# Performance work log

Measured on AMD Instinct MI355X. Metric: run time of the kernel, lower is better.

The kernel has to match this reference:

```python
import jax, jax.numpy as jnp
import numpy as np

K = 3  # dynamic filter kernel size
EPS = 1e-10


def _filter_norm_spatial(s, std_param):
    # s: (B, K*K, H, W); normalize over filter-tap dim (unbiased std, as torch)
    s = s - s.mean(axis=1, keepdims=True)
    s = s / (s.std(axis=1, keepdims=True, ddof=1) + EPS)
    return s * std_param[None, :, None, None]


def _filter_norm_channel(cf, std_param, B, C):
    # cf: (B, C*K*K); normalize over the K*K taps of each channel
    cf = cf.reshape(B, C, K * K)
    cf = cf - cf.mean(axis=2, keepdims=True)
    cf = cf / (cf.std(axis=2, keepdims=True, ddof=1) + EPS)
    cf = cf.reshape(B, C * K * K) * std_param[None, :]
    return cf.reshape(B, C, K * K)


def _ddf_pack(x, sw, sb, sstd, cw1, cb1, cw2, cb2, cstd):
    B, C, H, W = x.shape
    # spatial branch: 1x1 conv -> per-pixel K*K spatial filter
    s = jnp.einsum('bchw,oc->bohw', x, sw) + sb[None, :, None, None]
    s = _filter_norm_spatial(s, sstd)                      # (B, 9, H, W)
    # channel branch: GAP -> SE MLP -> per-channel K*K filter
    g = x.mean(axis=(2, 3))                                # (B, C)
    h = jax.nn.relu(g @ cw1.T + cb1)                       # (B, mid)
    cf = h @ cw2.T + cb2                                   # (B, C*9)
    cf = _filter_norm_channel(cf, cstd, B, C)              # (B, C, 9)
    # apply decoupled dynamic filter: w[b,c,uv,h,w] = cf[b,c,uv] * s[b,uv,h,w]
    pad = K // 2
    xp = jnp.pad(x, ((0, 0), (0, 0), (pad, pad), (pad, pad)))
    # patches: (B, C, 9, H, W) -- the 9 shifted views (unfold)
    patches = jnp.stack([xp[:, :, i:i + H, j:j + W]
                         for i in range(K) for j in range(K)], axis=2)
    return jnp.einsum('bckhw,bck,bkhw->bchw', patches, cf, s)


def setup_inputs() -> dict:
    key = jax.random.key(0)
    ks = jax.random.split(key, 20)
    nf, mid = 64, 12
    std_scale = np.sqrt(2.0) / K  # calculate_gain('relu') / kernel_size
    d = {'x': jax.random.normal(ks[0], (4, nf, 256, 256), jnp.float32)}
    i = 1
    for p in ('1', '2'):
        d['sw' + p] = jax.random.normal(ks[i], (K * K, nf), jnp.float32) * 0.1; i += 1
        d['sb' + p] = jax.random.normal(ks[i], (K * K,), jnp.float32) * 0.1; i += 1
        d['sstd' + p] = jax.random.normal(ks[i], (K * K,), jnp.float32) * std_scale; i += 1
        d['cw1_' + p] = jax.random.normal(ks[i], (mid, nf), jnp.float32) * 0.1; i += 1
        d['cb1_' + p] = jax.random.normal(ks[i], (mid,), jnp.float32) * 0.1; i += 1
        d['cw2_' + p] = jax.random.normal(ks[i], (nf * K * K, mid), jnp.float32) * 0.1; i += 1
        d['cb2_' + p] = jax.random.normal(ks[i], (nf * K * K,), jnp.float32) * 0.1; i += 1
        d['cstd' + p] = jax.random.normal(ks[i], (nf * K * K,), jnp.float32) * std_scale; i += 1
    return d


def reference(x, sw1, sb1, sstd1, cw1_1, cb1_1, cw2_1, cb2_1, cstd1,
              sw2, sb2, sstd2, cw1_2, cb1_2, cw2_2, cb2_2, cstd2):
    out = _ddf_pack(x, sw1, sb1, sstd1, cw1_1, cb1_1, cw2_1, cb2_1, cstd1)
    out = jax.nn.relu(out)
    out = _ddf_pack(out, sw2, sb2, sstd2, cw1_2, cb1_2, cw2_2, cb2_2, cstd2)
    return x + out
```

## Files before the change

kernel.cpp:

```cpp
#include <hip/hip_runtime.h>

#define B_ 4
#define C_ 64
#define H_ 256
#define W_ 256
#define HW_ (H_*W_)
#define MID_ 12
#define NPB_ 256

typedef _Float16 h4 __attribute__((ext_vector_type(4)));

__device__ __forceinline__ float wave_reduce64(float v) {
#pragma unroll
    for (int off = 32; off; off >>= 1) v += __shfl_xor(v, off, 64);
    return v;
}

__device__ __forceinline__ void fnorm4_store_pm(const float4* t9,
    const float* __restrict__ sstd, float* sp ) {
    float4 mean = make_float4(0, 0, 0, 0);
#pragma unroll
    for (int t = 0; t < 9; ++t) {
        mean.x += t9[t].x; mean.y += t9[t].y; mean.z += t9[t].z; mean.w += t9[t].w;
    }
    mean.x *= (1.f/9.f); mean.y *= (1.f/9.f); mean.z *= (1.f/9.f); mean.w *= (1.f/9.f);
    float4 var = make_float4(0, 0, 0, 0);
#pragma unroll
    for (int t = 0; t < 9; ++t) {
        float dx = t9[t].x - mean.x, dy = t9[t].y - mean.y;
        float dz = t9[t].z - mean.z, dw = t9[t].w - mean.w;
        var.x = fmaf(dx, dx, var.x); var.y = fmaf(dy, dy, var.y);
        var.z = fmaf(dz, dz, var.z); var.w = fmaf(dw, dw, var.w);
    }
    const float inv[4] = {
        1.f / (sqrtf(var.x * (1.f/8.f)) + 1e-10f),
        1.f / (sqrtf(var.y * (1.f/8.f)) + 1e-10f),
        1.f / (sqrtf(var.z * (1.f/8.f)) + 1e-10f),
        1.f / (sqrtf(var.w * (1.f/8.f)) + 1e-10f)};
    const float mn[4] = {mean.x, mean.y, mean.z, mean.w};
#pragma unroll
    for (int j = 0; j < 4; ++j) {
        float v9[9];
#pragma unroll
        for (int t = 0; t < 9; ++t) {
            float raw = (j == 0) ? t9[t].x : (j == 1) ? t9[t].y : (j == 2) ? t9[t].z : t9[t].w;
            v9[t] = (raw - mn[j]) * inv[j] * sstd[t];
        }
        float* o = sp + j * 12;
        *(float4*)(o)     = make_float4(v9[0], v9[1], v9[2], v9[3]);
        *(float4*)(o + 4) = make_float4(v9[4], v9[5], v9[6], v9[7]);
        *(float4*)(o + 8) = make_float4(v9[8], 0.f, 0.f, 0.f);
    }
}

template<bool HALF>
__global__ __launch_bounds__(256) void prep_kernel(const void* __restrict__ xin,
    const float* __restrict__ sw, const float* __restrict__ sb,
    const float* __restrict__ sstd, float* __restrict__ sarr, float* __restrict__ gp) {
    const int lane = threadIdx.x & 63, wv = threadIdx.x >> 6;
    const int row = blockIdx.x;
    const int b = blockIdx.y;
    const int c0 = wv * 16;
    const int pix = row * W_ + lane * 4;
    __shared__ float4 stl[3][9][64];

    float4 st[9];
#pragma unroll
    for (int t = 0; t < 9; ++t) st[t] = make_float4(0, 0, 0, 0);

    const size_t base = (size_t)b * C_ * HW_ + pix;
    const float* xbF = (const float*)xin + base;
    const _Float16* xbH = (const _Float16*)xin + base;

#define LOAD4(DST, CC) do {                                                   \
        if constexpr (HALF) {                                                 \
            h4 v_ = *(const h4*)(xbH + (size_t)(CC) * HW_);                   \
            DST = make_float4((float)v_[0], (float)v_[1],                     \
                              (float)v_[2], (float)v_[3]);                    \
        } else {                                                              \
            DST = *(const float4*)(xbF + (size_t)(CC) * HW_);                 \
        }                                                                     \
    } while (0)

#define PREP_COMP(BUF, CC) do {                                               \
        _Pragma("unroll")                                                     \
        for (int i_ = 0; i_ < 4; ++i_) {                                      \
            const int c_ = (CC) + i_;                                         \
            float4 v_ = BUF[i_];                                              \
            _Pragma("unroll")                                                 \
            for (int t_ = 0; t_ < 9; ++t_) {                                  \
                const float wt_ = sw[t_ * C_ + c_];                           \
                st[t_].x = fmaf(v_.x, wt_, st[t_].x);                         \
                st[t_].y = fmaf(v_.y, wt_, st[t_].y);                         \
                st[t_].z = fmaf(v_.z, wt_, st[t_].z);                         \
                st[t_].w = fmaf(v_.w, wt_, st[t_].w);                         \
            }                                                                 \
            float g_ = wave_reduce64(((v_.x + v_.y) + (v_.z + v_.w)));        \
            if (lane == 0) gp[((size_t)b * C_ + c_) * NPB_ + blockIdx.x] = g_; \
        }                                                                     \
    } while (0)

    float4 vA[4], vB[4];
#pragma unroll
    for (int i = 0; i < 4; ++i) LOAD4(vA[i], c0 + i);
#pragma unroll
    for (int k = 0; k < 16; k += 8) {
#pragma unroll
        for (int i = 0; i < 4; ++i) LOAD4(vB[i], c0 + k + 4 + i);
        PREP_COMP(vA, c0 + k);
        if (k + 8 < 16) {
#pragma unroll
            for (int i = 0; i < 4; ++i) LOAD4(vA[i], c0 + k + 8 + i);
        }
        PREP_COMP(vB, c0 + k + 4);
    }
#undef LOAD4
#undef PREP_COMP

    if (wv) {
#pragma unroll
        for (int t = 0; t < 9; ++t) stl[wv - 1][t][lane] = st[t];
    }
    __syncthreads();
    if (wv == 0) {
#pragma unroll
        for (int t = 0; t < 9; ++t) {
            float bb = sb[t];
#pragma unroll
            for (int j = 0; j < 3; ++j) {
                float4 o = stl[j][t][lane];
                st[t].x += o.x; st[t].y += o.y; st[t].z += o.z; st[t].w += o.w;
            }
            st[t].x += bb; st[t].y += bb; st[t].z += bb; st[t].w += bb;
        }
        fnorm4_store_pm(st, sstd, sarr + ((size_t)b * HW_ + pix) * 12);
    }
}

__global__ __launch_bounds__(256) void cfk(const float* __restrict__ gp,
    const float* __restrict__ cw1, const float* __restrict__ cb1,
    const float* __restrict__ cw2, const float* __restrict__ cb2,
    const float* __restrict__ cstd, float* __restrict__ cf) {
    const int tid = threadIdx.x;
    const int b = tid >> 6, c = tid & 63;
    __shared__ float gsm[B_][C_];
    __shared__ float hsm[B_][MID_];
    {
        const float4* p4 = (const float4*)(gp + ((size_t)b * C_ + c) * NPB_);
        float s = 0.f;
#pragma unroll 8
        for (int i = 0; i < NPB_ / 4; ++i) { float4 v = p4[i]; s += (v.x + v.y) + (v.z + v.w); }
        gsm[b][c] = s * (1.f / HW_);
    }
    __syncthreads();
    if (tid < B_ * MID_) {
        int b2 = tid / MID_, m = tid % MID_;
        float a = cb1[m];
        for (int cc = 0; cc < C_; ++cc) a = fmaf(gsm[b2][cc], cw1[m * C_ + cc], a);
        hsm[b2][m] = fmaxf(a, 0.f);
    }
    __syncthreads();
    float v[9];
    float mean = 0.f;
#pragma unroll
    for (int t = 0; t < 9; ++t) {
        int o = c * 9 + t;
        float a = cb2[o];
#pragma unroll
        for (int m = 0; m < MID_; ++m) a = fmaf(hsm[b][m], cw2[o * MID_ + m], a);
        v[t] = a;
        mean += a;
    }
    mean *= (1.f / 9.f);
    float var = 0.f;
#pragma unroll
    for (int t = 0; t < 9; ++t) { float d = v[t] - mean; var += d * d; }
    float inv = 1.f / (sqrtf(var * (1.f / 8.f)) + 1e-10f);
    float* o12 = cf + ((size_t)b * C_ + c) * 12;
#pragma unroll
    for (int t = 0; t < 9; ++t) o12[t] = (v[t] - mean) * inv * cstd[c * 9 + t];
    o12[9] = 0.f; o12[10] = 0.f; o12[11] = 0.f;
}

template<bool RELU, bool RESID, bool INH, bool OUTH>
__global__ __launch_bounds__(256) void apply_kernel(const void* __restrict__ in,
    const float* __restrict__ sarr, const float* __restrict__ cf,
    const float* __restrict__ resid, void* __restrict__ out) {
    const int lane = threadIdx.x & 63, wv = threadIdx.x >> 6;
    const int col = blockIdx.x * 64 + lane;
    const int row = blockIdx.y * 4 + wv;
    const int z = blockIdx.z;
    const int b = z >> 3;
    const int c0 = (z & 7) * 8;
    const int pix = row * W_ + col;

    float s0[9];
    int off9[9];
    {
        const float* sp = sarr + ((size_t)b * HW_ + pix) * 12;
        float4 a = *(const float4*)(sp);
        float4 b4 = *(const float4*)(sp + 4);
        float4 c4 = *(const float4*)(sp + 8);
        s0[0] = a.x; s0[1] = a.y; s0[2] = a.z; s0[3] = a.w;
        s0[4] = b4.x; s0[5] = b4.y; s0[6] = b4.z; s0[7] = b4.w;
        s0[8] = c4.x;
#pragma unroll
        for (int dr = -1; dr <= 1; ++dr)
#pragma unroll
            for (int dc = -1; dc <= 1; ++dc) {
                const int t = (dr + 1) * 3 + (dc + 1);
                const bool ok = (row + dr >= 0) && (row + dr < H_) &&
                                (col + dc >= 0) && (col + dc < W_);
                off9[t] = ok ? (pix + dr * W_ + dc) : pix;
                if (!ok) s0[t] = 0.f;
            }
    }

    const size_t cbase = ((size_t)b * C_ + c0) * HW_;
    const float* inF = (const float*)in + cbase;
    const _Float16* inH = (const _Float16*)in + cbase;
    const float* cfb = cf + ((size_t)b * C_ + c0) * 12;
    const float* rb  = RESID ? ((const float*)resid + cbase + pix) : nullptr;
    float* outF = (float*)out + cbase + pix;
    _Float16* outH = (_Float16*)out + cbase + pix;

    float m0[9], m1[9], m2[9], m3[9];
    float rv0 = 0.f, rv1 = 0.f, rv2 = 0.f, rv3 = 0.f;

#define LD9(M, RV, cc) do {                                                  \
        if constexpr (INH) {                                                 \
            const _Float16* p_ = inH + (size_t)(cc) * HW_;                   \
            _Pragma("unroll")                                                \
            for (int t_ = 0; t_ < 9; ++t_) M[t_] = (float)p_[off9[t_]];      \
        } else {                                                             \
            const float* p_ = inF + (size_t)(cc) * HW_;                      \
            _Pragma("unroll")                                                \
            for (int t_ = 0; t_ < 9; ++t_) M[t_] = p_[off9[t_]];             \
        }                                                                    \
        if (RESID) RV = rb[(size_t)(cc) * HW_];                              \
    } while (0)

#define CP9(M, RV, cc) do {                                                  \
        const float* cfc_ = cfb + (size_t)(cc) * 12;                         \
        float acc_ = 0.f;                                                    \
        _Pragma("unroll")                                                    \
        for (int t_ = 0; t_ < 9; ++t_)                                       \
            acc_ = fmaf(M[t_] * s0[t_], cfc_[t_], acc_);                     \
        float o_ = RELU ? fmaxf(acc_, 0.f) : acc_;                           \
        if (RESID) o_ += RV;                                                 \
        if constexpr (OUTH) outH[(size_t)(cc) * HW_] = (_Float16)o_;         \
        else                outF[(size_t)(cc) * HW_] = o_;                   \
    } while (0)

    LD9(m0, rv0, 0); LD9(m1, rv1, 1); LD9(m2, rv2, 2); LD9(m3, rv3, 3);
    CP9(m0, rv0, 0); LD9(m0, rv0, 4);
    CP9(m1, rv1, 1); LD9(m1, rv1, 5);
    CP9(m2, rv2, 2); LD9(m2, rv2, 6);
    CP9(m3, rv3, 3); LD9(m3, rv3, 7);
    CP9(m0, rv0, 4); CP9(m1, rv1, 5); CP9(m2, rv2, 6); CP9(m3, rv3, 7);
#undef LD9
#undef CP9
}

extern "C" void kernel_launch(void* const* d_in, const int* in_sizes, int n_in,
                              void* d_out, int out_size, void* d_ws, size_t ws_size,
                              hipStream_t stream) {
    const float* x     = (const float*)d_in[0];
    const float* sw1   = (const float*)d_in[1];
    const float* sb1   = (const float*)d_in[2];
    const float* sstd1 = (const float*)d_in[3];
    const float* cw1_1 = (const float*)d_in[4];
    const float* cb1_1 = (const float*)d_in[5];
    const float* cw2_1 = (const float*)d_in[6];
    const float* cb2_1 = (const float*)d_in[7];
    const float* cstd1 = (const float*)d_in[8];
    const float* sw2   = (const float*)d_in[9];
    const float* sb2   = (const float*)d_in[10];
    const float* sstd2 = (const float*)d_in[11];
    const float* cw1_2 = (const float*)d_in[12];
    const float* cb1_2 = (const float*)d_in[13];
    const float* cw2_2 = (const float*)d_in[14];
    const float* cb2_2 = (const float*)d_in[15];
    const float* cstd2 = (const float*)d_in[16];
    float* outp = (float*)d_out;

    const size_t n_out1 = (size_t)B_ * C_ * HW_;
    const size_t n_s    = (size_t)B_ * HW_ * 12;
    const size_t n_cf   = (size_t)B_ * C_ * 12;
    const size_t n_gp   = (size_t)B_ * C_ * NPB_;
    const size_t need = n_out1 * sizeof(_Float16)
                      + (2 * n_s + 2 * n_cf + 2 * n_gp) * sizeof(float);
    if (ws_size < need) return;

    _Float16* out1h = (_Float16*)d_ws;
    float* s1  = (float*)((char*)d_ws + n_out1 * sizeof(_Float16));
    float* s2  = s1 + n_s;
    float* cf1 = s2 + n_s;
    float* cf2 = cf1 + n_cf;
    float* gp1 = cf2 + n_cf;
    float* gp2 = gp1 + n_gp;

    dim3 gprep(H_, B_);
    dim3 gapply(W_ / 64, H_ / 4, B_ * 8);

    prep_kernel<false><<<gprep, 256, 0, stream>>>(x, sw1, sb1, sstd1, s1, gp1);
    cfk<<<1, 256, 0, stream>>>(gp1, cw1_1, cb1_1, cw2_1, cb2_1, cstd1, cf1);
    apply_kernel<true, false, false, true><<<gapply, 256, 0, stream>>>(
        x, s1, cf1, nullptr, out1h);
    prep_kernel<true><<<gprep, 256, 0, stream>>>(out1h, sw2, sb2, sstd2, s2, gp2);
    cfk<<<1, 256, 0, stream>>>(gp2, cw1_2, cb1_2, cw2_2, cb2_2, cstd2, cf2);
    apply_kernel<false, true, true, false><<<gapply, 256, 0, stream>>>(
        out1h, s2, cf2, x, outp);
}
```

Measured before the change: 140.1 us.

## Compute two adjacent pixels per thread in apply kernel with vectorized loads

Each thread in the apply kernel now handles two horizontally adjacent pixels and four channels instead of one pixel and eight. Overlapping stencil taps are shared, so 12 loads per channel (three paired center loads plus left and right edges) replace 18 scalar gathers for two pixels. Outputs and residuals use paired stores and loads. Boundary handling moves to per-row and per-column flags. The change reduces load instruction count and improves coalescing width, while per-thread channel reuse of the spatial filter drops from eight to four channels.

```diff
diff --git a/kernel.cpp b/kernel.cpp
--- a/kernel.cpp
+++ b/kernel.cpp
@@ -9,6 +9,7 @@
 #define NPB_ 256
 
 typedef _Float16 h4 __attribute__((ext_vector_type(4)));
+typedef _Float16 h2 __attribute__((ext_vector_type(2)));
 
 __device__ __forceinline__ float wave_reduce64(float v) {
 #pragma unroll
@@ -187,33 +188,50 @@
     const float* __restrict__ sarr, const float* __restrict__ cf,
     const float* __restrict__ resid, void* __restrict__ out) {
     const int lane = threadIdx.x & 63, wv = threadIdx.x >> 6;
-    const int col = blockIdx.x * 64 + lane;
+    const int col0 = blockIdx.x * 128 + lane * 2;
     const int row = blockIdx.y * 4 + wv;
     const int z = blockIdx.z;
-    const int b = z >> 3;
-    const int c0 = (z & 7) * 8;
-    const int pix = row * W_ + col;
-
-    float s0[9];
-    int off9[9];
+    const int b = z >> 4;
+    const int c0 = (z & 15) * 4;
+    const int pix = row * W_ + col0;
+
+    const bool rup = row > 0, rdn = row < H_ - 1;
+    const bool cl = col0 > 0;
+    const bool cr = (col0 + 1) < (W_ - 1);
+
+    float s0a[9], s0b[9];
     {
         const float* sp = sarr + ((size_t)b * HW_ + pix) * 12;
-        float4 a = *(const float4*)(sp);
-        float4 b4 = *(const float4*)(sp + 4);
-        float4 c4 = *(const float4*)(sp + 8);
-        s0[0] = a.x; s0[1] = a.y; s0[2] = a.z; s0[3] = a.w;
-        s0[4] = b4.x; s0[5] = b4.y; s0[6] = b4.z; s0[7] = b4.w;
-        s0[8] = c4.x;
-#pragma unroll
-        for (int dr = -1; dr <= 1; ++dr)
-#pragma unroll
-            for (int dc = -1; dc <= 1; ++dc) {
-                const int t = (dr + 1) * 3 + (dc + 1);
-                const bool ok = (row + dr >= 0) && (row + dr < H_) &&
-                                (col + dc >= 0) && (col + dc < W_);
-                off9[t] = ok ? (pix + dr * W_ + dc) : pix;
-                if (!ok) s0[t] = 0.f;
-            }
+        float4 q0 = *(const float4*)(sp);
+        float4 q1 = *(const float4*)(sp + 4);
+        float4 q2 = *(const float4*)(sp + 8);
+        float4 q3 = *(const float4*)(sp + 12);
+        float4 q4 = *(const float4*)(sp + 16);
+        float4 q5 = *(const float4*)(sp + 20);
+        s0a[0] = q0.x; s0a[1] = q0.y; s0a[2] = q0.z; s0a[3] = q0.w;
+        s0a[4] = q1.x; s0a[5] = q1.y; s0a[6] = q1.z; s0a[7] = q1.w;
+        s0a[8] = q2.x;
+        s0b[0] = q3.x; s0b[1] = q3.y; s0b[2] = q3.z; s0b[3] = q3.w;
+        s0b[4] = q4.x; s0b[5] = q4.y; s0b[6] = q4.z; s0b[7] = q4.w;
+        s0b[8] = q5.x;
+#pragma unroll
+        for (int t = 0; t < 3; ++t) {
+            if (!rup) { s0a[t] = 0.f; s0b[t] = 0.f; }
+            if (!rdn) { s0a[t + 6] = 0.f; s0b[t + 6] = 0.f; }
+        }
+        if (!cl) { s0a[0] = 0.f; s0a[3] = 0.f; s0a[6] = 0.f; }
+        if (!cr) { s0b[2] = 0.f; s0b[5] = 0.f; s0b[8] = 0.f; }
+    }
+
+    int offM[3], offL[3], offR[3];
+    {
+        const int ro[3] = {rup ? -W_ : 0, 0, rdn ? W_ : 0};
+#pragma unroll
+        for (int dr = 0; dr < 3; ++dr) {
+            offM[dr] = pix + ro[dr];
+            offL[dr] = offM[dr] + (cl ? -1 : 0);
+            offR[dr] = offM[dr] + (cr ? 2 : 0);
+        }
     }
 
     const size_t cbase = ((size_t)b * C_ + c0) * HW_;
@@ -224,42 +242,56 @@
     float* outF = (float*)out + cbase + pix;
     _Float16* outH = (_Float16*)out + cbase + pix;
 
-    float m0[9], m1[9], m2[9], m3[9];
-    float rv0 = 0.f, rv1 = 0.f, rv2 = 0.f, rv3 = 0.f;
-
-#define LD9(M, RV, cc) do {                                                  \
-        if constexpr (INH) {                                                 \
-            const _Float16* p_ = inH + (size_t)(cc) * HW_;                   \
-            _Pragma("unroll")                                                \
-            for (int t_ = 0; t_ < 9; ++t_) M[t_] = (float)p_[off9[t_]];      \
-        } else {                                                             \
-            const float* p_ = inF + (size_t)(cc) * HW_;                      \
-            _Pragma("unroll")                                                \
-            for (int t_ = 0; t_ < 9; ++t_) M[t_] = p_[off9[t_]];             \
-        }                                                                    \
-        if (RESID) RV = rb[(size_t)(cc) * HW_];                              \
-    } while (0)
-
-#define CP9(M, RV, cc) do {                                                  \
-        const float* cfc_ = cfb + (size_t)(cc) * 12;                         \
-        float acc_ = 0.f;                                                    \
-        _Pragma("unroll")                                                    \
-        for (int t_ = 0; t_ < 9; ++t_)                                       \
-            acc_ = fmaf(M[t_] * s0[t_], cfc_[t_], acc_);                     \
-        float o_ = RELU ? fmaxf(acc_, 0.f) : acc_;                           \
-        if (RESID) o_ += RV;                                                 \
-        if constexpr (OUTH) outH[(size_t)(cc) * HW_] = (_Float16)o_;         \
-        else                outF[(size_t)(cc) * HW_] = o_;                   \
-    } while (0)
-
-    LD9(m0, rv0, 0); LD9(m1, rv1, 1); LD9(m2, rv2, 2); LD9(m3, rv3, 3);
-    CP9(m0, rv0, 0); LD9(m0, rv0, 4);
-    CP9(m1, rv1, 1); LD9(m1, rv1, 5);
-    CP9(m2, rv2, 2); LD9(m2, rv2, 6);
-    CP9(m3, rv3, 3); LD9(m3, rv3, 7);
-    CP9(m0, rv0, 4); CP9(m1, rv1, 5); CP9(m2, rv2, 6); CP9(m3, rv3, 7);
-#undef LD9
-#undef CP9
+    float mm[4][3][2], ll[4][3], rr[4][3];
+    float2 rv[4];
+
+#pragma unroll
+    for (int c = 0; c < 4; ++c) {
+        if constexpr (INH) {
+            const _Float16* p = inH + (size_t)c * HW_;
+#pragma unroll
+            for (int dr = 0; dr < 3; ++dr) {
+                h2 mv = *(const h2*)(p + offM[dr]);
+                mm[c][dr][0] = (float)mv[0]; mm[c][dr][1] = (float)mv[1];
+                ll[c][dr] = (float)p[offL[dr]];
+                rr[c][dr] = (float)p[offR[dr]];
+            }
+        } else {
+            const float* p = inF + (size_t)c * HW_;
+#pragma unroll
+            for (int dr = 0; dr < 3; ++dr) {
+                float2 mv = *(const float2*)(p + offM[dr]);
+                mm[c][dr][0] = mv.x; mm[c][dr][1] = mv.y;
+                ll[c][dr] = p[offL[dr]];
+                rr[c][dr] = p[offR[dr]];
+            }
+        }
+        if (RESID) rv[c] = *(const float2*)(rb + (size_t)c * HW_);
+    }
+
+#pragma unroll
+    for (int c = 0; c < 4; ++c) {
+        const float* cfc = cfb + (size_t)c * 12;
+        float a0 = 0.f, a1 = 0.f;
+#pragma unroll
+        for (int dr = 0; dr < 3; ++dr) {
+            const int t = dr * 3;
+            a0 = fmaf(ll[c][dr]    * s0a[t],     cfc[t],     a0);
+            a0 = fmaf(mm[c][dr][0] * s0a[t + 1], cfc[t + 1], a0);
+            a0 = fmaf(mm[c][dr][1] * s0a[t + 2], cfc[t + 2], a0);
+            a1 = fmaf(mm[c][dr][0] * s0b[t],     cfc[t],     a1);
+            a1 = fmaf(mm[c][dr][1] * s0b[t + 1], cfc[t + 1], a1);
+            a1 = fmaf(rr[c][dr]    * s0b[t + 2], cfc[t + 2], a1);
+        }
+        if (RELU) { a0 = fmaxf(a0, 0.f); a1 = fmaxf(a1, 0.f); }
+        if (RESID) { a0 += rv[c].x; a1 += rv[c].y; }
+        if constexpr (OUTH) {
+            h2 o; o[0] = (_Float16)a0; o[1] = (_Float16)a1;
+            *(h2*)(outH + (size_t)c * HW_) = o;
+        } else {
+            *(float2*)(outF + (size_t)c * HW_) = make_float2(a0, a1);
+        }
+    }
 }
 
 extern "C" void kernel_launch(void* const* d_in, const int* in_sizes, int n_in,
@@ -301,7 +333,7 @@
     float* gp2 = gp1 + n_gp;
 
     dim3 gprep(H_, B_);
-    dim3 gapply(W_ / 64, H_ / 4, B_ * 8);
+    dim3 gapply(2, H_ / 4, B_ * 16);
 
     prep_kernel<false><<<gprep, 256, 0, stream>>>(x, sw1, sb1, sstd1, s1, gp1);
     cfk<<<1, 256, 0, stream>>>(gp1, cw1_1, cb1_1, cw2_1, cb2_1, cstd1, cf1);
```

New measurement: 163.7 us. 16.8% more time.
